# Kernel optimization log

Measured on AMD Instinct MI355X. Metric: run time of the kernel, lower is better.

The kernel has to match this reference:

```python
import jax, jax.numpy as jnp
import numpy as np

B, C, H, W, NW = 4, 32, 64, 64, 64
VMAX = 1.0


def _sunflower_mu_stddev(n, vmax, alpha=1.0):
    # sunflower seed arrangement on the complex plane (matches torch source)
    b = np.round(alpha * np.sqrt(n))
    phi = (np.sqrt(5.0) + 1.0) * 0.5
    k = np.arange(1, n + 1, dtype=np.float64)
    r = np.where(k > n - b, 1.0, np.sqrt(k - 0.5) / np.sqrt(n - (b + 1.0) / 2.0))
    theta = 2.0 * np.pi * k / phi ** 2
    mu = (r * np.cos(theta) + 1j * r * np.sin(theta)) * vmax
    # nearest-neighbor distance (replaces sklearn NearestNeighbors exactly)
    X = np.stack((mu.real, mu.imag), -1)  # (n,2)
    D = np.linalg.norm(X[:, None, :] - X[None, :, :], axis=-1)
    np.fill_diagonal(D, np.inf)
    nn_d = D.min(axis=1)
    stddev = (nn_d * nn_d).astype(np.float32)
    return mu.real.astype(np.float32), mu.imag.astype(np.float32), stddev


def setup_inputs() -> dict:
    key = jax.random.key(0)
    k1, k2, k3, k4 = jax.random.split(key, 4)
    mu_r, mu_i, stddev = _sunflower_mu_stddev(NW, VMAX)
    return {
        "x_real": jax.random.normal(k1, (B, C, H, W), dtype=jnp.float32),
        "x_imag": jax.random.normal(k2, (B, C, H, W), dtype=jnp.float32),
        "w_real": jax.random.normal(k3, (C, NW), dtype=jnp.float32) * 0.1,
        "w_imag": jax.random.normal(k4, (C, NW), dtype=jnp.float32) * 0.1,
        "b_real": jnp.zeros((1, C, 1), dtype=jnp.float32),
        "b_imag": jnp.zeros((1, C, 1), dtype=jnp.float32),
        "mu_real": jnp.asarray(mu_r),
        "mu_imag": jnp.asarray(mu_i),
        "stddev": jnp.asarray(stddev),
    }


def reference(x_real, x_imag, w_real, w_imag, b_real, b_imag, mu_real, mu_imag, stddev):
    Bb, Cc, Hh, Ww = x_real.shape
    # (B,C,HW,1) complex input vs (1,1,1,NW) complex centers
    xr = x_real.reshape(Bb, Cc, -1, 1)
    xi = x_imag.reshape(Bb, Cc, -1, 1)
    dr = xr - mu_real.reshape(1, 1, 1, -1)
    di = xi - mu_imag.reshape(1, 1, 1, -1)
    # conj(dist)*dist = |dist|^2 (real); exp of it is real-valued
    rbf = jnp.exp(-(dr * dr + di * di) / (2.0 * stddev))  # (B,C,HW,NW) real
    # complex channel-weighted reduction + complex bias
    out_r = jnp.einsum('abcd,bd->abc', rbf, w_real) + b_real
    out_i = jnp.einsum('abcd,bd->abc', rbf, w_imag) + b_imag
    # return real/imag stacked on last axis: (B,C,H,W,2)
    out = jnp.stack([out_r.reshape(Bb, Cc, Hh, Ww), out_i.reshape(Bb, Cc, Hh, Ww)], axis=-1)
    return out
```

## Files before the change

### kernel.cpp

```cpp
#include <hip/hip_runtime.h>

#define NB 4
#define NC 32
#define HW 4096
#define NW 64

#define PPT 4
#define TPB 256
#define PPB (PPT * TPB)
#define TILES (HW / PPB)

__global__ __launch_bounds__(TPB) void rbf_kernel(
    const float* __restrict__ x_real, const float* __restrict__ x_imag,
    const float* __restrict__ w_real, const float* __restrict__ w_imag,
    const float* __restrict__ b_real, const float* __restrict__ b_imag,
    const float* __restrict__ mu_real, const float* __restrict__ mu_imag,
    const float* __restrict__ stddev, float* __restrict__ out)
{
    const int bc   = blockIdx.x / TILES;
    const int tile = blockIdx.x % TILES;
    const int c    = bc % NC;
    const int t    = threadIdx.x;

    __shared__ float s_mu_r[NW], s_mu_i[NW], s_coef[NW], s_wr[NW], s_wi[NW];
    if (t < NW) {
        s_mu_r[t] = mu_real[t];
        s_mu_i[t] = mu_imag[t];
        s_coef[t] = -1.4426950408889634f / (2.0f * stddev[t]);
        s_wr[t]   = w_real[c * NW + t];
        s_wi[t]   = w_imag[c * NW + t];
    }
    __syncthreads();

    const int base = bc * HW + tile * PPB + t;

    float xr[PPT], xi[PPT], ar[PPT], ai[PPT];
#pragma unroll
    for (int p = 0; p < PPT; ++p) {
        xr[p] = x_real[base + p * TPB];
        xi[p] = x_imag[base + p * TPB];
        ar[p] = 0.0f;
        ai[p] = 0.0f;
    }

#pragma unroll 8
    for (int k = 0; k < NW; ++k) {
        const float mr = s_mu_r[k];
        const float mi = s_mu_i[k];
        const float cf = s_coef[k];
        const float wr = s_wr[k];
        const float wi = s_wi[k];
#pragma unroll
        for (int p = 0; p < PPT; ++p) {
            float dr  = xr[p] - mr;
            float di  = xi[p] - mi;
            float d2  = fmaf(di, di, dr * dr);
            float rbf = __builtin_amdgcn_exp2f(d2 * cf);
            ar[p] = fmaf(rbf, wr, ar[p]);
            ai[p] = fmaf(rbf, wi, ai[p]);
        }
    }

    const float br = b_real[c];
    const float bi = b_imag[c];
    float2* __restrict__ out2 = reinterpret_cast<float2*>(out);
#pragma unroll
    for (int p = 0; p < PPT; ++p) {
        out2[base + p * TPB] = make_float2(ar[p] + br, ai[p] + bi);
    }
}

extern "C" void kernel_launch(void* const* d_in, const int* in_sizes, int n_in,
                              void* d_out, int out_size, void* d_ws, size_t ws_size,
                              hipStream_t stream) {
    const float* x_real  = (const float*)d_in[0];
    const float* x_imag  = (const float*)d_in[1];
    const float* w_real  = (const float*)d_in[2];
    const float* w_imag  = (const float*)d_in[3];
    const float* b_real  = (const float*)d_in[4];
    const float* b_imag  = (const float*)d_in[5];
    const float* mu_real = (const float*)d_in[6];
    const float* mu_imag = (const float*)d_in[7];
    const float* stddev  = (const float*)d_in[8];
    float* out = (float*)d_out;

    const int grid = NB * NC * TILES;
    rbf_kernel<<<grid, TPB, 0, stream>>>(x_real, x_imag, w_real, w_imag,
                                         b_real, b_imag, mu_real, mu_imag,
                                         stddev, out);
}
```

Measured before the change: 78.72 us.

## Expand squared distance algebraically with precomputed tables and vectorize IO

Adds a small prep kernel that writes per-center coefficients (cf, -2cf*mu_r, -2cf*mu_i, cf*|mu|^2) and packed interleaved weights into workspace. The exponent then becomes three FMAs on the precomputed |x|^2 instead of subtract/multiply/FMA/multiply. The main kernel also drops shared memory and the barrier, reading the tables through uniform global loads. Loads and stores are now float4 with contiguous pixels per thread. The trade-off is an extra kernel launch and possible cancellation error when |x| is large relative to mu.

```diff
diff --git a/kernel.cpp b/kernel.cpp
--- a/kernel.cpp
+++ b/kernel.cpp
@@ -10,64 +10,75 @@
 #define PPB (PPT * TPB)
 #define TILES (HW / PPB)
 
-__global__ __launch_bounds__(TPB) void rbf_kernel(
+__global__ __launch_bounds__(TPB) void rbf_prep(
+    const float* __restrict__ w_real, const float* __restrict__ w_imag,
+    const float* __restrict__ mu_real, const float* __restrict__ mu_imag,
+    const float* __restrict__ stddev,
+    float4* __restrict__ tab, float2* __restrict__ wtab)
+{
+    const int t = blockIdx.x * blockDim.x + threadIdx.x;
+    if (t < NW) {
+        const float cf = -1.4426950408889634f / (2.0f * stddev[t]);
+        const float mr = mu_real[t];
+        const float mi = mu_imag[t];
+        tab[t] = make_float4(cf, -2.0f * cf * mr, -2.0f * cf * mi,
+                             cf * (mr * mr + mi * mi));
+    }
+    if (t < NC * NW) {
+        wtab[t] = make_float2(w_real[t], w_imag[t]);
+    }
+}
+
+__global__ __launch_bounds__(TPB) void rbf_main(
     const float* __restrict__ x_real, const float* __restrict__ x_imag,
-    const float* __restrict__ w_real, const float* __restrict__ w_imag,
     const float* __restrict__ b_real, const float* __restrict__ b_imag,
-    const float* __restrict__ mu_real, const float* __restrict__ mu_imag,
-    const float* __restrict__ stddev, float* __restrict__ out)
+    const float4* __restrict__ tab, const float2* __restrict__ wtab,
+    float* __restrict__ out)
 {
     const int bc   = blockIdx.x / TILES;
     const int tile = blockIdx.x % TILES;
-    const int c    = bc % NC;
+    const int c    = bc & (NC - 1);
     const int t    = threadIdx.x;
 
-    __shared__ float s_mu_r[NW], s_mu_i[NW], s_coef[NW], s_wr[NW], s_wi[NW];
-    if (t < NW) {
-        s_mu_r[t] = mu_real[t];
-        s_mu_i[t] = mu_imag[t];
-        s_coef[t] = -1.4426950408889634f / (2.0f * stddev[t]);
-        s_wr[t]   = w_real[c * NW + t];
-        s_wi[t]   = w_imag[c * NW + t];
-    }
-    __syncthreads();
+    const int blockBase = bc * HW + tile * PPB;
 
-    const int base = bc * HW + tile * PPB + t;
+    const float4 xr4 = reinterpret_cast<const float4*>(x_real + blockBase)[t];
+    const float4 xi4 = reinterpret_cast<const float4*>(x_imag + blockBase)[t];
+    const float xr[PPT] = {xr4.x, xr4.y, xr4.z, xr4.w};
+    const float xi[PPT] = {xi4.x, xi4.y, xi4.z, xi4.w};
 
-    float xr[PPT], xi[PPT], ar[PPT], ai[PPT];
+    float n2[PPT];
 #pragma unroll
-    for (int p = 0; p < PPT; ++p) {
-        xr[p] = x_real[base + p * TPB];
-        xi[p] = x_imag[base + p * TPB];
-        ar[p] = 0.0f;
-        ai[p] = 0.0f;
-    }
+    for (int p = 0; p < PPT; ++p)
+        n2[p] = fmaf(xr[p], xr[p], xi[p] * xi[p]);
+
+    const float br = b_real[c];
+    const float bi = b_imag[c];
+
+    float ar[PPT], ai[PPT];
+#pragma unroll
+    for (int p = 0; p < PPT; ++p) { ar[p] = br; ai[p] = bi; }
+
+    const float2* __restrict__ wrow = wtab + c * NW;
 
 #pragma unroll 8
     for (int k = 0; k < NW; ++k) {
-        const float mr = s_mu_r[k];
-        const float mi = s_mu_i[k];
-        const float cf = s_coef[k];
-        const float wr = s_wr[k];
-        const float wi = s_wi[k];
+        const float4 row = tab[k];
+        const float2 w   = wrow[k];
 #pragma unroll
         for (int p = 0; p < PPT; ++p) {
-            float dr  = xr[p] - mr;
-            float di  = xi[p] - mi;
-            float d2  = fmaf(di, di, dr * dr);
-            float rbf = __builtin_amdgcn_exp2f(d2 * cf);
-            ar[p] = fmaf(rbf, wr, ar[p]);
-            ai[p] = fmaf(rbf, wi, ai[p]);
+            float e = fmaf(row.x, n2[p], row.w);
+            e = fmaf(row.y, xr[p], e);
+            e = fmaf(row.z, xi[p], e);
+            const float r = __builtin_amdgcn_exp2f(e);
+            ar[p] = fmaf(r, w.x, ar[p]);
+            ai[p] = fmaf(r, w.y, ai[p]);
         }
     }
 
-    const float br = b_real[c];
-    const float bi = b_imag[c];
-    float2* __restrict__ out2 = reinterpret_cast<float2*>(out);
-#pragma unroll
-    for (int p = 0; p < PPT; ++p) {
-        out2[base + p * TPB] = make_float2(ar[p] + br, ai[p] + bi);
-    }
+    float4* __restrict__ out4 = reinterpret_cast<float4*>(out + 2 * blockBase);
+    out4[2 * t + 0] = make_float4(ar[0], ai[0], ar[1], ai[1]);
+    out4[2 * t + 1] = make_float4(ar[2], ai[2], ar[3], ai[3]);
 }
 
 extern "C" void kernel_launch(void* const* d_in, const int* in_sizes, int n_in,
@@ -84,8 +95,13 @@
     const float* stddev  = (const float*)d_in[8];
     float* out = (float*)d_out;
 
+    float4* tab  = (float4*)d_ws;
+    float2* wtab = (float2*)((char*)d_ws + NW * sizeof(float4));
+
+    rbf_prep<<<(NC * NW + TPB - 1) / TPB, TPB, 0, stream>>>(
+        w_real, w_imag, mu_real, mu_imag, stddev, tab, wtab);
+
     const int grid = NB * NC * TILES;
-    rbf_kernel<<<grid, TPB, 0, stream>>>(x_real, x_imag, w_real, w_imag,
-                                         b_real, b_imag, mu_real, mu_imag,
-                                         stddev, out);
+    rbf_main<<<grid, TPB, 0, stream>>>(x_real, x_imag, b_real, b_imag,
+                                       tab, wtab, out);
 }
```

Result: no change. 78.97 us (+0.3%).
